# Kernel optimization log

Measured on AMD Instinct MI355X. Metric: run time of the kernel, lower is better.

## Reference

```python
import jax, jax.numpy as jnp
import numpy as np

L, D_MODEL, D_INNER, DT_RANK, D_STATE, D_CONV, VOCAB = 4, 768, 1536, 48, 16, 4, 32000
B, S = 1, 1024


def rmsnorm(x, w, eps=1e-5):
    return x * jax.lax.rsqrt(jnp.mean(x * x, axis=-1, keepdims=True) + eps) * w


def causal_depthwise_conv(x, w, b):
    # x: [B,S,D]; w: [D,1,K] (torch Conv1d groups=D weight layout); causal left-pad K-1
    y = jax.lax.conv_general_dilated(
        x.transpose(0, 2, 1), w, window_strides=(1,), padding=[(D_CONV - 1, 0)],
        dimension_numbers=('NCH', 'OIH', 'NCH'), feature_group_count=D_INNER)
    return y.transpose(0, 2, 1) + b


def selective_scan(u, dt, A, Bm, Cm, Dv):
    # Faithful to the source: A_delta = exp(dt (x) A), clamp(min=-20) is a no-op on exp output
    A_delta = jnp.clip(jnp.exp(jnp.einsum('bld,dn->bldn', dt, A)), -20.0, None)
    B_delta_u = jnp.einsum('bld,bld,bln->bldn', dt, u, Bm)
    shifted = jnp.pad(A_delta[:, 1:], ((0, 0), (1, 0), (0, 0), (0, 0)))
    A_cum = jnp.exp(jnp.cumsum(shifted, axis=1))
    h = B_delta_u / (A_cum + 1e-12)
    y = jnp.einsum('bldn,bln->bld', jnp.cumsum(h, axis=1) * A_cum, Cm)
    return y + u * Dv


def setup_inputs() -> dict:
    key = jax.random.key(0)
    ks = jax.random.split(key, 8)
    return {
        'tokens': jax.random.randint(ks[0], (B, S), 0, VOCAB),
        'embedding': jax.random.normal(ks[1], (VOCAB, D_MODEL), jnp.float32) * 0.02,
        'norm_w': jnp.ones((L, D_MODEL), jnp.float32),
        'in_proj_w': jax.random.normal(ks[2], (L, 2 * D_INNER, D_MODEL), jnp.float32) * 0.02,
        'conv_w': jax.random.normal(ks[3], (L, D_INNER, 1, D_CONV), jnp.float32) * 0.2,
        'conv_b': jnp.zeros((L, D_INNER), jnp.float32),
        'x_proj_w': jax.random.normal(ks[4], (L, DT_RANK + 2 * D_STATE, D_INNER), jnp.float32) * 0.02,
        'dt_proj_w': jax.random.normal(ks[5], (L, D_INNER, DT_RANK), jnp.float32) * 0.001,
        'dt_proj_b': jnp.full((L, D_INNER), 5.0, jnp.float32),  # delta~5 keeps exp(cumsum(exp(dt*A))) finite
        'A_log': jnp.tile(jnp.log(jnp.arange(1, D_STATE + 1, dtype=jnp.float32)), (L, D_INNER, 1)),
        'D_skip': jnp.ones((L, D_INNER), jnp.float32),
        'out_proj_w': jax.random.normal(ks[6], (L, D_MODEL, D_INNER), jnp.float32) * 0.02,
        'final_norm_w': jnp.ones((D_MODEL,), jnp.float32),
    }


def reference(tokens, embedding, norm_w, in_proj_w, conv_w, conv_b, x_proj_w,
              dt_proj_w, dt_proj_b, A_log, D_skip, out_proj_w, final_norm_w):
    x = embedding[tokens]  # [B,S,d_model]
    for i in range(L):
        h = rmsnorm(x, norm_w[i])
        xz = h @ in_proj_w[i].T                      # [B,S,2*d_inner]
        xi, res = xz[..., :D_INNER], xz[..., D_INNER:]
        xi = jax.nn.silu(causal_depthwise_conv(xi, conv_w[i], conv_b[i]))
        proj = xi @ x_proj_w[i].T                    # [B,S,dt_rank+2*d_state]
        dt = jax.nn.softplus(proj[..., :DT_RANK] @ dt_proj_w[i].T + dt_proj_b[i])
        Bm = proj[..., DT_RANK:DT_RANK + D_STATE]
        Cm = proj[..., DT_RANK + D_STATE:]
        A = -jnp.exp(A_log[i])                       # [d_inner, d_state]
        y = selective_scan(xi, dt, A, Bm, Cm, D_skip[i])
        x = x + (y * jax.nn.silu(res)) @ out_proj_w[i].T
    return rmsnorm(x, final_norm_w) @ embedding.T    # tied LM head: [B,S,vocab]
```

## Files before the change

### kernel.cpp

```cpp
#include <hip/hip_runtime.h>
#include <hip/hip_bf16.h>
#include <cmath>

namespace {

constexpr int kL      = 4;
constexpr int kDModel = 768;
constexpr int kDInner = 1536;
constexpr int kDtRank = 48;
constexpr int kDState = 16;
constexpr int kDConv  = 4;
constexpr int kSeq    = 1024;
constexpr int kPLd    = 96;
constexpr int kVocab  = 32000;
constexpr int kCH     = 64;
constexpr int kNCH    = kSeq / kCH;
constexpr int kDN     = kDInner * kDState;

using short8 = __attribute__((ext_vector_type(8))) short;
using f32x4  = __attribute__((ext_vector_type(4))) float;

__device__ __forceinline__ float silu_f(float v) {
    return v / (1.f + __expf(-v));
}

__device__ __forceinline__ void split_bf16(float v, __hip_bfloat16& hi, __hip_bfloat16& lo) {
    hi = __float2bfloat16(v);
    lo = __float2bfloat16(v - __bfloat162float(hi));
}

__global__ void __launch_bounds__(256) f2b_kernel(
    const float* __restrict__ src, __hip_bfloat16* __restrict__ dst, int n) {
    int i = (blockIdx.x * 256 + threadIdx.x) * 4;
    const int stride = gridDim.x * 256 * 4;
    for (; i + 3 < n; i += stride) {
        const float4 v = *reinterpret_cast<const float4*>(src + i);
        dst[i + 0] = __float2bfloat16(v.x);
        dst[i + 1] = __float2bfloat16(v.y);
        dst[i + 2] = __float2bfloat16(v.z);
        dst[i + 3] = __float2bfloat16(v.w);
    }
}

__global__ void __launch_bounds__(256) split3_kernel(
    const float* __restrict__ src, int ldsrc, int rows, int cols,
    __hip_bfloat16* __restrict__ dst, int rowsPad) {
    const int idx = blockIdx.x * 256 + threadIdx.x;
    if (idx >= rowsPad * cols) return;
    const int r = idx / cols, c = idx % cols;
    const float v = (r < rows) ? src[(size_t)r * ldsrc + c] : 0.f;
    __hip_bfloat16 hi, lo;
    split_bf16(v, hi, lo);
    __hip_bfloat16* row = dst + (size_t)r * 3 * cols;
    row[c] = hi; row[cols + c] = hi; row[2 * cols + c] = lo;
}

__global__ void __launch_bounds__(256) embed_kernel(
    const int* __restrict__ tokens, const float* __restrict__ emb,
    float* __restrict__ x) {
    const int s = blockIdx.x;
    const int t = tokens[s];
    const float* src = emb + (size_t)t * kDModel;
    float* dst = x + (size_t)s * kDModel;
    for (int d = threadIdx.x; d < kDModel; d += blockDim.x) dst[d] = src[d];
}

template <bool SPLIT>
__global__ void __launch_bounds__(256) rmsnorm_kernel(
    const float* __restrict__ x, const float* __restrict__ w,
    __hip_bfloat16* __restrict__ out) {
    const int s = blockIdx.x;
    const float* row = x + (size_t)s * kDModel;
    float ss = 0.f;
    for (int d = threadIdx.x; d < kDModel; d += blockDim.x) {
        const float v = row[d];
        ss = fmaf(v, v, ss);
    }
    #pragma unroll
    for (int m = 32; m; m >>= 1) ss += __shfl_xor(ss, m);
    __shared__ float red[4];
    if ((threadIdx.x & 63) == 0) red[threadIdx.x >> 6] = ss;
    __syncthreads();
    const float total = red[0] + red[1] + red[2] + red[3];
    const float scale = rsqrtf(total / (float)kDModel + 1e-5f);
    __hip_bfloat16* dst = out + (size_t)s * (SPLIT ? 3 * kDModel : kDModel);
    for (int d = threadIdx.x; d < kDModel; d += blockDim.x) {
        const float v = row[d] * scale * w[d];
        if (SPLIT) {
            __hip_bfloat16 hi, lo;
            split_bf16(v, hi, lo);
            dst[d] = hi; dst[kDModel + d] = lo; dst[2 * kDModel + d] = hi;
        } else {
            dst[d] = __float2bfloat16(v);
        }
    }
}

template <int BM, int BN, int KSPLIT>
__global__ void __launch_bounds__(256) mfma_gemm(
    const __hip_bfloat16* __restrict__ A, int lda,
    const __hip_bfloat16* __restrict__ B, int ldb,
    float* __restrict__ C, int ldc,
    int N, int K, size_t partStride) {
    constexpr int BK = 32;
    __shared__ unsigned short As[BM * BK];
    __shared__ unsigned short Bs[BN * BK];
    const int tid  = threadIdx.x;
    const int lane = tid & 63;

    const int nwg = gridDim.x * gridDim.y;
    int bid = blockIdx.y * gridDim.x + blockIdx.x;
    {
        const int q = nwg >> 3, r = nwg & 7;
        const int xcd = bid & 7, pos = bid >> 3;
        bid = (xcd < r ? xcd * (q + 1) : r * (q + 1) + (xcd - r) * q) + pos;
    }
    const int m0 = (bid % gridDim.x) * BM;
    const int n0 = (bid / gridDim.x) * BN;

    const int Kp = K / KSPLIT;
    const int kbeg = (KSPLIT > 1) ? blockIdx.z * Kp : 0;
    float* Cw = (KSPLIT > 1) ? C + (size_t)blockIdx.z * partStride : C;
    constexpr int WM = BM / 2, WN = BN / 2;
    constexpr int MR = WM / 16, NR = WN / 16;
    const int wave = tid >> 6;
    const int wm = (wave >> 1) * WM, wn = (wave & 1) * WN;
    const int l15 = lane & 15, l4 = lane >> 4;
    f32x4 acc[MR][NR] = {};

    for (int kk = 0; kk < Kp; kk += BK) {
        const int k0 = kbeg + kk;
        for (int idx = tid; idx < BM * 4; idx += 256) {
            const int r = idx >> 2, q = idx & 3;
            const int qs = q ^ ((r >> 1) & 3);
            __builtin_amdgcn_global_load_lds(
                (const __attribute__((address_space(1))) void*)(A + (size_t)(m0 + r) * lda + k0 + qs * 8),
                (__attribute__((address_space(3))) void*)(As + (idx - lane) * 8),
                16, 0, 0);
        }
        for (int idx = tid; idx < BN * 4; idx += 256) {
            const int r = idx >> 2, q = idx & 3;
            const int qs = q ^ ((r >> 1) & 3);
            __builtin_amdgcn_global_load_lds(
                (const __attribute__((address_space(1))) void*)(B + (size_t)(n0 + r) * ldb + k0 + qs * 8),
                (__attribute__((address_space(3))) void*)(Bs + (idx - lane) * 8),
                16, 0, 0);
        }
        __syncthreads();

        short8 af[MR], bfv[NR];
        #pragma unroll
        for (int mi = 0; mi < MR; ++mi) {
            const int R = wm + mi * 16 + l15;
            af[mi] = *reinterpret_cast<const short8*>(&As[(R * 4 + (l4 ^ ((R >> 1) & 3))) * 8]);
        }
        #pragma unroll
        for (int ni = 0; ni < NR; ++ni) {
            const int R = wn + ni * 16 + l15;
            bfv[ni] = *reinterpret_cast<const short8*>(&Bs[(R * 4 + (l4 ^ ((R >> 1) & 3))) * 8]);
        }
        #pragma unroll
        for (int mi = 0; mi < MR; ++mi)
            #pragma unroll
            for (int ni = 0; ni < NR; ++ni)
                acc[mi][ni] = __builtin_amdgcn_mfma_f32_16x16x32_bf16(
                    af[mi], bfv[ni], acc[mi][ni], 0, 0, 0);
        __syncthreads();
    }

    #pragma unroll
    for (int mi = 0; mi < MR; ++mi) {
        const int mrow = m0 + wm + mi * 16 + l4 * 4;
        #pragma unroll
        for (int ni = 0; ni < NR; ++ni) {
            const int ncol = n0 + wn + ni * 16 + l15;
            if (ncol >= N) continue;
            #pragma unroll
            for (int r = 0; r < 4; ++r)
                Cw[(size_t)(mrow + r) * ldc + ncol] = acc[mi][ni][r];
        }
    }
}

template <int NP, bool ADD>
__global__ void __launch_bounds__(256) reduce_parts(
    const float* __restrict__ parts, size_t stride,
    float* __restrict__ dst, int count) {
    const int i = (blockIdx.x * 256 + threadIdx.x) * 4;
    if (i >= count) return;
    float4 s = *reinterpret_cast<const float4*>(parts + i);
    #pragma unroll
    for (int p = 1; p < NP; ++p) {
        const float4 v = *reinterpret_cast<const float4*>(parts + (size_t)p * stride + i);
        s.x += v.x; s.y += v.y; s.z += v.z; s.w += v.w;
    }
    float4* d = reinterpret_cast<float4*>(dst + i);
    if (ADD) {
        float4 o = *d;
        o.x += s.x; o.y += s.y; o.z += s.z; o.w += s.w;
        *d = o;
    } else {
        *d = s;
    }
}

__global__ void __launch_bounds__(256) dt_kernel(
    const float* __restrict__ proj, const float* __restrict__ dtw,
    const float* __restrict__ bias, float* __restrict__ dt) {
    __shared__ float sw[kDtRank][257];
    const int tid = threadIdx.x;
    const int n0 = blockIdx.x * 256;
    const int m0 = blockIdx.y * 8;
    for (int idx = tid; idx < 256 * kDtRank; idx += 256) {
        const int nn = idx / kDtRank, k = idx % kDtRank;
        sw[k][nn] = dtw[(size_t)(n0 + nn) * kDtRank + k];
    }
    __syncthreads();
    const int n = n0 + tid;
    const float b = bias[n];
    #pragma unroll
    for (int mi = 0; mi < 8; ++mi) {
        const float* pr = proj + (size_t)(m0 + mi) * kPLd;
        float acc = b;
        #pragma unroll
        for (int k = 0; k < kDtRank; ++k)
            acc = fmaf(pr[k], sw[k][tid], acc);
        acc = (acc > 20.f) ? acc : log1pf(__expf(acc));
        dt[(size_t)(m0 + mi) * kDInner + n] = acc;
    }
}

__global__ void __launch_bounds__(256) conv_silu_kernel(
    const float* __restrict__ p0, const float* __restrict__ p1,
    const float* __restrict__ cw, const float* __restrict__ cb,
    float* __restrict__ xi, __hip_bfloat16* __restrict__ xi2) {
    const int s = blockIdx.x;
    const int d = blockIdx.y * 256 + threadIdx.x;
    float acc = cb[d];
    #pragma unroll
    for (int k = 0; k < kDConv; ++k) {
        const int sl = s - (kDConv - 1) + k;
        if (sl >= 0) {
            const size_t off = (size_t)sl * (2 * kDInner) + d;
            acc = fmaf(p0[off] + p1[off], cw[d * kDConv + k], acc);
        }
    }
    const float v = silu_f(acc);
    xi[(size_t)s * kDInner + d] = v;
    __hip_bfloat16 hi, lo;
    split_bf16(v, hi, lo);
    __hip_bfloat16* row = xi2 + (size_t)s * 3 * kDInner;
    row[d] = hi; row[kDInner + d] = lo; row[2 * kDInner + d] = hi;
}

__global__ void __launch_bounds__(256) scan_part1(
    const float* __restrict__ dt, const float* __restrict__ u,
    const float* __restrict__ proj, const float* __restrict__ A_log,
    float* __restrict__ P, float* __restrict__ S) {
    __shared__ float sdt[kCH][16], su[kCH][16], sB[kCH][16];
    const int tid = threadIdx.x;
    const int n = tid & 15, dl = tid >> 4;
    const int d0 = blockIdx.x * 16;
    const int l0 = blockIdx.y * kCH;
    for (int idx = tid; idx < kCH * 16; idx += 256) {
        const int r = idx >> 4, c = idx & 15;
        sdt[r][c] = dt[(size_t)(l0 + r) * kDInner + d0 + c];
        su [r][c] = u [(size_t)(l0 + r) * kDInner + d0 + c];
        sB [r][c] = proj[(size_t)(l0 + r) * kPLd + kDtRank + c];
    }
    __syncthreads();
    const int d = d0 + dl;
    const float Adn = -__expf(A_log[d * kDState + n]);
    float state = 0.f, sumA = 0.f;
    #pragma unroll 8
    for (int l = 0; l < kCH; ++l) {
        const float dtv = sdt[l][dl];
        const float adelta = __expf(dtv * Adn);
        const float mult = __expf(adelta);
        state = fmaf(state, mult, dtv * su[l][dl] * sB[l][n]);
        sumA += adelta;
    }
    const int dn = d * kDState + n;
    P[(size_t)blockIdx.y * kDN + dn] = __expf(sumA);
    S[(size_t)blockIdx.y * kDN + dn] = state;
}

__global__ void __launch_bounds__(256) scan_combine(
    const float* __restrict__ P, const float* __restrict__ S,
    float* __restrict__ SI) {
    const int dn = blockIdx.x * 256 + threadIdx.x;
    float s = 0.f;
    #pragma unroll
    for (int j = 0; j < kNCH; ++j) {
        const size_t idx = (size_t)j * kDN + dn;
        SI[idx] = s;
        s = fmaf(s, P[idx], S[idx]);
    }
}

__global__ void __launch_bounds__(256) scan_part2(
    const float* __restrict__ dt, const float* __restrict__ u,
    const float* __restrict__ proj, const float* __restrict__ A_log,
    const float* __restrict__ D_skip, const float* __restrict__ SI,
    float* __restrict__ y) {
    __shared__ float sdt[kCH][16], su[kCH][16], sB[kCH][16], sC[kCH][16];
    __shared__ float sy[kCH][16];
    const int tid = threadIdx.x;
    const int n = tid & 15, dl = tid >> 4;
    const int d0 = blockIdx.x * 16;
    const int l0 = blockIdx.y * kCH;
    for (int idx = tid; idx < kCH * 16; idx += 256) {
        const int r = idx >> 4, c = idx & 15;
        sdt[r][c] = dt[(size_t)(l0 + r) * kDInner + d0 + c];
        su [r][c] = u [(size_t)(l0 + r) * kDInner + d0 + c];
        sB [r][c] = proj[(size_t)(l0 + r) * kPLd + kDtRank + c];
        sC [r][c] = proj[(size_t)(l0 + r) * kPLd + kDtRank + kDState + c];
    }
    __syncthreads();
    const int d = d0 + dl;
    const float Adn = -__expf(A_log[d * kDState + n]);
    const float Dv  = D_skip[d];
    float state = SI[(size_t)blockIdx.y * kDN + d * kDState + n];
    for (int l = 0; l < kCH; ++l) {
        const float dtv = sdt[l][dl];
        const float uv  = su[l][dl];
        const float mult = __expf(__expf(dtv * Adn));
        state = fmaf(state, mult, dtv * uv * sB[l][n]);
        float contrib = state * sC[l][n];
        contrib += __shfl_xor(contrib, 8);
        contrib += __shfl_xor(contrib, 4);
        contrib += __shfl_xor(contrib, 2);
        contrib += __shfl_xor(contrib, 1);
        if (n == 0) sy[l][dl] = fmaf(uv, Dv, contrib);
    }
    __syncthreads();
    for (int idx = tid; idx < kCH * 16; idx += 256) {
        const int r = idx >> 4, c = idx & 15;
        y[(size_t)(l0 + r) * kDInner + d0 + c] = sy[r][c];
    }
}

__global__ void __launch_bounds__(256) mul_silu_kernel(
    const float* __restrict__ y, const float* __restrict__ p0,
    const float* __restrict__ p1, __hip_bfloat16* __restrict__ g2) {
    const int s = blockIdx.x;
    const int d = blockIdx.y * 256 + threadIdx.x;
    const size_t off = (size_t)s * (2 * kDInner) + kDInner + d;
    const float res = p0[off] + p1[off];
    const float v = y[(size_t)s * kDInner + d] * silu_f(res);
    __hip_bfloat16 hi, lo;
    split_bf16(v, hi, lo);
    __hip_bfloat16* row = g2 + (size_t)s * 3 * kDInner;
    row[d] = hi; row[kDInner + d] = lo; row[2 * kDInner + d] = hi;
}

}

extern "C" void kernel_launch(void* const* d_in, const int* in_sizes, int n_in,
                              void* d_out, int out_size, void* d_ws, size_t ws_size,
                              hipStream_t stream) {
    const int*   tokens       = (const int*)d_in[0];
    const float* embedding    = (const float*)d_in[1];
    const float* norm_w       = (const float*)d_in[2];
    const float* in_proj_w    = (const float*)d_in[3];
    const float* conv_w       = (const float*)d_in[4];
    const float* conv_b       = (const float*)d_in[5];
    const float* x_proj_w     = (const float*)d_in[6];
    const float* dt_proj_w    = (const float*)d_in[7];
    const float* dt_proj_b    = (const float*)d_in[8];
    const float* A_log        = (const float*)d_in[9];
    const float* D_skip       = (const float*)d_in[10];
    const float* out_proj_w   = (const float*)d_in[11];
    const float* final_norm_w = (const float*)d_in[12];
    float* out = (float*)d_out;

    constexpr int K3m = 3 * kDModel;
    constexpr int K3i = 3 * kDInner;

    char* ws = (char*)d_ws;
    auto alloc = [&](size_t bytes) { char* p = ws; ws += (bytes + 255) & ~(size_t)255; return p; };
    float* x    = (float*)alloc((size_t)kSeq * kDModel * 4);
    float* xi   = (float*)alloc((size_t)kSeq * kDInner * 4);
    float* proj = (float*)alloc((size_t)kSeq * kPLd * 4);
    float* dt   = (float*)alloc((size_t)kSeq * kDInner * 4);
    float* y    = (float*)alloc((size_t)kSeq * kDInner * 4);
    float* scanP  = (float*)alloc((size_t)kNCH * kDN * 4);
    float* scanS  = (float*)alloc((size_t)kNCH * kDN * 4);
    float* scanSI = (float*)alloc((size_t)kNCH * kDN * 4);
    float* partsXZ = (float*)alloc((size_t)2 * kSeq * 2 * kDInner * 4);
    float* partsP  = (float*)alloc((size_t)8 * kSeq * kPLd * 4);
    float* partsO  = (float*)alloc((size_t)4 * kSeq * kDModel * 4);
    __hip_bfloat16* h_bf   = (__hip_bfloat16*)alloc((size_t)kSeq * kDModel * 2);
    __hip_bfloat16* h2     = (__hip_bfloat16*)alloc((size_t)kSeq * K3m * 2);
    __hip_bfloat16* xi2    = (__hip_bfloat16*)alloc((size_t)kSeq * K3i * 2);
    __hip_bfloat16* g2     = (__hip_bfloat16*)alloc((size_t)kSeq * K3i * 2);
    __hip_bfloat16* emb_bf = (__hip_bfloat16*)alloc((size_t)kVocab * kDModel * 2);
    __hip_bfloat16* inw2   = (__hip_bfloat16*)alloc((size_t)kL * 2 * kDInner * K3m * 2);
    __hip_bfloat16* outw2  = (__hip_bfloat16*)alloc((size_t)kL * kDModel * K3i * 2);
    __hip_bfloat16* xw2    = (__hip_bfloat16*)alloc((size_t)kL * kPLd * K3i * 2);

    f2b_kernel<<<4096, 256, 0, stream>>>(embedding, emb_bf, kVocab * kDModel);
    split3_kernel<<<(kL * 2 * kDInner * kDModel + 255) / 256, 256, 0, stream>>>(
        in_proj_w, kDModel, kL * 2 * kDInner, kDModel, inw2, kL * 2 * kDInner);
    split3_kernel<<<(kL * kDModel * kDInner + 255) / 256, 256, 0, stream>>>(
        out_proj_w, kDInner, kL * kDModel, kDInner, outw2, kL * kDModel);
    for (int i = 0; i < kL; ++i)
        split3_kernel<<<(kPLd * kDInner + 255) / 256, 256, 0, stream>>>(
            x_proj_w + (size_t)i * (kDtRank + 2 * kDState) * kDInner, kDInner,
            kDtRank + 2 * kDState, kDInner, xw2 + (size_t)i * kPLd * K3i, kPLd);

    embed_kernel<<<kSeq, 256, 0, stream>>>(tokens, embedding, x);

    for (int i = 0; i < kL; ++i) {
        rmsnorm_kernel<true><<<kSeq, 256, 0, stream>>>(x, norm_w + (size_t)i * kDModel, h2);

        mfma_gemm<128, 128, 2><<<dim3(kSeq / 128, 2 * kDInner / 128, 2), 256, 0, stream>>>(
            h2, K3m, inw2 + (size_t)i * 2 * kDInner * K3m, K3m,
            partsXZ, 2 * kDInner, 2 * kDInner, K3m, (size_t)kSeq * 2 * kDInner);

        conv_silu_kernel<<<dim3(kSeq, kDInner / 256), 256, 0, stream>>>(
            partsXZ, partsXZ + (size_t)kSeq * 2 * kDInner,
            conv_w + (size_t)i * kDInner * kDConv, conv_b + (size_t)i * kDInner,
            xi, xi2);

        mfma_gemm<128, 96, 8><<<dim3(kSeq / 128, 1, 8), 256, 0, stream>>>(
            xi2, K3i, xw2 + (size_t)i * kPLd * K3i, K3i,
            partsP, kPLd, kPLd, K3i, (size_t)kSeq * kPLd);
        reduce_parts<8, false><<<(kSeq * kPLd / 4 + 255) / 256, 256, 0, stream>>>(
            partsP, (size_t)kSeq * kPLd, proj, kSeq * kPLd);

        dt_kernel<<<dim3(kDInner / 256, kSeq / 8), 256, 0, stream>>>(
            proj, dt_proj_w + (size_t)i * kDInner * kDtRank,
            dt_proj_b + (size_t)i * kDInner, dt);

        const float* A_l = A_log + (size_t)i * kDInner * kDState;
        scan_part1<<<dim3(kDInner / 16, kNCH), 256, 0, stream>>>(
            dt, xi, proj, A_l, scanP, scanS);
        scan_combine<<<kDN / 256, 256, 0, stream>>>(scanP, scanS, scanSI);
        scan_part2<<<dim3(kDInner / 16, kNCH), 256, 0, stream>>>(
            dt, xi, proj, A_l, D_skip + (size_t)i * kDInner, scanSI, y);

        mul_silu_kernel<<<dim3(kSeq, kDInner / 256), 256, 0, stream>>>(
            y, partsXZ, partsXZ + (size_t)kSeq * 2 * kDInner, g2);

        mfma_gemm<128, 128, 4><<<dim3(kSeq / 128, kDModel / 128, 4), 256, 0, stream>>>(
            g2, K3i, outw2 + (size_t)i * kDModel * K3i, K3i,
            partsO, kDModel, kDModel, K3i, (size_t)kSeq * kDModel);
        reduce_parts<4, true><<<(kSeq * kDModel / 4 + 255) / 256, 256, 0, stream>>>(
            partsO, (size_t)kSeq * kDModel, x, kSeq * kDModel);
    }

    rmsnorm_kernel<false><<<kSeq, 256, 0, stream>>>(x, final_norm_w, h_bf);
    mfma_gemm<128, 128, 1><<<dim3(kSeq / 128, kVocab / 128, 1), 256, 0, stream>>>(
        h_bf, kDModel, emb_bf, kDModel, out, kVocab, kVocab, kDModel, 0);
}
```

Measured before the change: 901.1 us.

## Double-buffer GEMM LDS staging and widen x_proj GEMM to 128 with 16-way split-K

The MFMA GEMM now uses two LDS buffers, issuing async global-to-LDS loads for the next K tile before computing on the current one. Full __syncthreads calls are replaced by explicit vmcnt/lgkmcnt waits plus s_barrier. The x_proj weights are padded to 128 rows so that GEMM can use the 128x128 tile, and its split-K rises from 8 to 16, which doubles the partial buffers and the work in the reduce step. The aim is to hide global load latency behind MFMA work, at the cost of twice the LDS per block, which may lower occupancy. The correctness of the padded weight rows depends on split3 zero-filling them.

Result: faster. 851.7 us (-5.5%).

```diff
diff --git a/kernel.cpp b/kernel.cpp
--- a/kernel.cpp
+++ b/kernel.cpp
@@ -12,6 +12,7 @@
 constexpr int kDConv  = 4;
 constexpr int kSeq    = 1024;
 constexpr int kPLd    = 96;
+constexpr int kPB     = 128;
 constexpr int kVocab  = 32000;
 constexpr int kCH     = 64;
 constexpr int kNCH    = kSeq / kCH;
@@ -103,8 +104,9 @@
     float* __restrict__ C, int ldc,
     int N, int K, size_t partStride) {
     constexpr int BK = 32;
-    __shared__ unsigned short As[BM * BK];
-    __shared__ unsigned short Bs[BN * BK];
+    static_assert(BM == 128 && BN == 128, "staging assumes 128x128");
+    __shared__ unsigned short As[2][BM * BK];
+    __shared__ unsigned short Bs[2][BN * BK];
     const int tid  = threadIdx.x;
     const int lane = tid & 63;
 
@@ -128,36 +130,51 @@
     const int l15 = lane & 15, l4 = lane >> 4;
     f32x4 acc[MR][NR] = {};
 
-    for (int kk = 0; kk < Kp; kk += BK) {
-        const int k0 = kbeg + kk;
-        for (int idx = tid; idx < BM * 4; idx += 256) {
-            const int r = idx >> 2, q = idx & 3;
-            const int qs = q ^ ((r >> 1) & 3);
+    auto stage = [&](int buf, int k0) {
+        #pragma unroll
+        for (int i = 0; i < 2; ++i) {
+            const int idx = tid + i * 256;
+            const int r = idx >> 2, qv = idx & 3;
+            const int qs = qv ^ ((r >> 1) & 3);
             __builtin_amdgcn_global_load_lds(
                 (const __attribute__((address_space(1))) void*)(A + (size_t)(m0 + r) * lda + k0 + qs * 8),
-                (__attribute__((address_space(3))) void*)(As + (idx - lane) * 8),
+                (__attribute__((address_space(3))) void*)(&As[buf][(idx - lane) * 8]),
                 16, 0, 0);
         }
-        for (int idx = tid; idx < BN * 4; idx += 256) {
-            const int r = idx >> 2, q = idx & 3;
-            const int qs = q ^ ((r >> 1) & 3);
+        #pragma unroll
+        for (int i = 0; i < 2; ++i) {
+            const int idx = tid + i * 256;
+            const int r = idx >> 2, qv = idx & 3;
+            const int qs = qv ^ ((r >> 1) & 3);
             __builtin_amdgcn_global_load_lds(
                 (const __attribute__((address_space(1))) void*)(B + (size_t)(n0 + r) * ldb + k0 + qs * 8),
-                (__attribute__((address_space(3))) void*)(Bs + (idx - lane) * 8),
+                (__attribute__((address_space(3))) void*)(&Bs[buf][(idx - lane) * 8]),
                 16, 0, 0);
         }
-        __syncthreads();
+    };
+
+    const int nt = Kp / BK;
+    int cur = 0;
+    stage(0, kbeg);
+    for (int t = 0; t < nt; ++t) {
+        if (t + 1 < nt) {
+            stage(cur ^ 1, kbeg + (t + 1) * BK);
+            asm volatile("s_waitcnt vmcnt(4)" ::: "memory");
+        } else {
+            asm volatile("s_waitcnt vmcnt(0)" ::: "memory");
+        }
+        __builtin_amdgcn_s_barrier();
 
         short8 af[MR], bfv[NR];
         #pragma unroll
         for (int mi = 0; mi < MR; ++mi) {
             const int R = wm + mi * 16 + l15;
-            af[mi] = *reinterpret_cast<const short8*>(&As[(R * 4 + (l4 ^ ((R >> 1) & 3))) * 8]);
+            af[mi] = *reinterpret_cast<const short8*>(&As[cur][(R * 4 + (l4 ^ ((R >> 1) & 3))) * 8]);
         }
         #pragma unroll
         for (int ni = 0; ni < NR; ++ni) {
             const int R = wn + ni * 16 + l15;
-            bfv[ni] = *reinterpret_cast<const short8*>(&Bs[(R * 4 + (l4 ^ ((R >> 1) & 3))) * 8]);
+            bfv[ni] = *reinterpret_cast<const short8*>(&Bs[cur][(R * 4 + (l4 ^ ((R >> 1) & 3))) * 8]);
         }
         #pragma unroll
         for (int mi = 0; mi < MR; ++mi)
@@ -165,7 +182,10 @@
             for (int ni = 0; ni < NR; ++ni)
                 acc[mi][ni] = __builtin_amdgcn_mfma_f32_16x16x32_bf16(
                     af[mi], bfv[ni], acc[mi][ni], 0, 0, 0);
-        __syncthreads();
+
+        asm volatile("s_waitcnt lgkmcnt(0)" ::: "memory");
+        __builtin_amdgcn_s_barrier();
+        cur ^= 1;
     }
 
     #pragma unroll
@@ -388,7 +408,7 @@
     float* scanS  = (float*)alloc((size_t)kNCH * kDN * 4);
     float* scanSI = (float*)alloc((size_t)kNCH * kDN * 4);
     float* partsXZ = (float*)alloc((size_t)2 * kSeq * 2 * kDInner * 4);
-    float* partsP  = (float*)alloc((size_t)8 * kSeq * kPLd * 4);
+    float* partsP  = (float*)alloc((size_t)16 * kSeq * kPLd * 4);
     float* partsO  = (float*)alloc((size_t)4 * kSeq * kDModel * 4);
     __hip_bfloat16* h_bf   = (__hip_bfloat16*)alloc((size_t)kSeq * kDModel * 2);
     __hip_bfloat16* h2     = (__hip_bfloat16*)alloc((size_t)kSeq * K3m * 2);
@@ -397,7 +417,7 @@
     __hip_bfloat16* emb_bf = (__hip_bfloat16*)alloc((size_t)kVocab * kDModel * 2);
     __hip_bfloat16* inw2   = (__hip_bfloat16*)alloc((size_t)kL * 2 * kDInner * K3m * 2);
     __hip_bfloat16* outw2  = (__hip_bfloat16*)alloc((size_t)kL * kDModel * K3i * 2);
-    __hip_bfloat16* xw2    = (__hip_bfloat16*)alloc((size_t)kL * kPLd * K3i * 2);
+    __hip_bfloat16* xw2    = (__hip_bfloat16*)alloc((size_t)kL * kPB * K3i * 2);
 
     f2b_kernel<<<4096, 256, 0, stream>>>(embedding, emb_bf, kVocab * kDModel);
     split3_kernel<<<(kL * 2 * kDInner * kDModel + 255) / 256, 256, 0, stream>>>(
@@ -405,9 +425,9 @@
     split3_kernel<<<(kL * kDModel * kDInner + 255) / 256, 256, 0, stream>>>(
         out_proj_w, kDInner, kL * kDModel, kDInner, outw2, kL * kDModel);
     for (int i = 0; i < kL; ++i)
-        split3_kernel<<<(kPLd * kDInner + 255) / 256, 256, 0, stream>>>(
+        split3_kernel<<<(kPB * kDInner + 255) / 256, 256, 0, stream>>>(
             x_proj_w + (size_t)i * (kDtRank + 2 * kDState) * kDInner, kDInner,
-            kDtRank + 2 * kDState, kDInner, xw2 + (size_t)i * kPLd * K3i, kPLd);
+            kDtRank + 2 * kDState, kDInner, xw2 + (size_t)i * kPB * K3i, kPB);
 
     embed_kernel<<<kSeq, 256, 0, stream>>>(tokens, embedding, x);
 
@@ -423,10 +443,10 @@
             conv_w + (size_t)i * kDInner * kDConv, conv_b + (size_t)i * kDInner,
             xi, xi2);
 
-        mfma_gemm<128, 96, 8><<<dim3(kSeq / 128, 1, 8), 256, 0, stream>>>(
-            xi2, K3i, xw2 + (size_t)i * kPLd * K3i, K3i,
+        mfma_gemm<128, 128, 16><<<dim3(kSeq / 128, 1, 16), 256, 0, stream>>>(
+            xi2, K3i, xw2 + (size_t)i * kPB * K3i, K3i,
             partsP, kPLd, kPLd, K3i, (size_t)kSeq * kPLd);
-        reduce_parts<8, false><<<(kSeq * kPLd / 4 + 255) / 256, 256, 0, stream>>>(
+        reduce_parts<16, false><<<(kSeq * kPLd / 4 + 255) / 256, 256, 0, stream>>>(
             partsP, (size_t)kSeq * kPLd, proj, kSeq * kPLd);
 
         dt_kernel<<<dim3(kDInner / 256, kSeq / 8), 256, 0, stream>>>(
```
